# Kernel tuning notes

Hardware: AMD Instinct MI355X
Metric: run time of the kernel (lower is better)

## Reference

```python
import jax, jax.numpy as jnp
import numpy as np

N_NODES = 32768
N_EDGES = 262144
N_TYPES = 10
EMB = 16            # node_embedding_size, irreps_node_in = 16x0e
NB = 20             # num_basis = conv_radius * basis_density_per_A
RADIUS = 5.0        # conv_radius
S, V, T = 16, 4, 2  # output multiplicities for 0e, 1o, 2e
HID = 64
SILU_NORM = 1.679177  # e3nn normalize2mom constant for silu (E[silu(z)^2]^-0.5)


def _sph_harm(u):
    # e3nn real spherical harmonics, lmax=2, component normalization, unit input
    x, y, z = u[:, 0], u[:, 1], u[:, 2]
    sh0 = jnp.ones_like(x)[:, None]
    sh1 = np.sqrt(3.0) * u  # [E,3]
    s15 = np.sqrt(15.0)
    sh2 = jnp.stack([
        s15 * x * z,
        s15 * x * y,
        np.sqrt(5.0) * (y * y - 0.5 * (x * x + z * z)),
        s15 * y * z,
        (s15 / 2.0) * (z * z - x * x),
    ], axis=-1)  # [E,5]
    return jnp.concatenate([sh0, sh1, sh2], axis=-1)  # [E,9]


def _radial_emb(dist):
    # e3nn soft_one_hot_linspace, basis='smooth_finite', cutoff=True
    centers = np.linspace(0.0, RADIUS, NB + 2)[1:-1].astype(np.float32)
    step = centers[1] - centers[0]
    d = (dist[:, None] - centers) / step  # [E,NB]
    mask = jnp.abs(d) < 1.0
    ds = jnp.where(mask, d, 0.0)
    # 1.14136 * exp(2) * exp(-1/(1+d)) * exp(-1/(1-d)) inside |d|<1, else 0
    f = 1.14136 * jnp.exp(2.0 - 1.0 / (1.0 + ds) - 1.0 / (1.0 - ds))
    return jnp.where(mask, f, 0.0) * np.sqrt(float(NB))  # .mul(num_basis**0.5)


def setup_inputs() -> dict:
    key = jax.random.key(0)
    ks = jax.random.split(key, 7)
    x = jax.random.uniform(ks[0], (N_NODES, N_TYPES), dtype=jnp.float32)
    pos = jax.random.uniform(ks[1], (N_NODES, 3), dtype=jnp.float32) * 4.0
    edge_index = jax.random.randint(ks[2], (2, N_EDGES), 0, N_NODES)
    W_emb1 = jax.random.normal(ks[3], (N_TYPES, HID), dtype=jnp.float32)
    W_emb2 = jax.random.normal(ks[4], (HID, EMB), dtype=jnp.float32)
    W_tp1 = jax.random.normal(ks[5], (NB, HID), dtype=jnp.float32)
    W_tp2 = jax.random.normal(ks[6], (HID, EMB * (S + V + T)), dtype=jnp.float32)
    return {"x": x, "pos": pos, "edge_index": edge_index,
            "W_emb1": W_emb1, "W_emb2": W_emb2, "W_tp1": W_tp1, "W_tp2": W_tp2}


def reference(x, pos, edge_index, W_emb1, W_emb2, W_tp1, W_tp2):
    # e3nn FullyConnectedNet (act=None): pure linear with 1/sqrt(fan_in)
    node_emb = ((x @ W_emb1) / np.sqrt(float(N_TYPES))) @ W_emb2 / np.sqrt(float(HID))  # [N,16]

    src, dst = edge_index[0], edge_index[1]
    vec = pos[dst] - pos[src]                                   # [E,3]
    dist = jnp.sqrt(jnp.sum(vec * vec, axis=1) + 1e-12)         # [E]
    unit = vec / dist[:, None]

    sh = _sph_harm(unit)        # [E,9]
    demb = _radial_emb(dist)    # [E,NB]

    # e3nn FullyConnectedNet with normalized silu on hidden layer
    h = SILU_NORM * jax.nn.silu((demb @ W_tp1) / np.sqrt(float(NB)))
    w = (h @ W_tp2) / np.sqrt(float(HID))  # [E, 352] per-edge TP weights

    E = w.shape[0]
    Ws = w[:, : EMB * S].reshape(E, EMB, S)
    Wv = w[:, EMB * S: EMB * (S + V)].reshape(E, EMB, V)
    Wt = w[:, EMB * (S + V):].reshape(E, EMB, T)

    z = node_emb[src]            # [E,16] gathered source scalars
    inv = 1.0 / np.sqrt(float(EMB))  # path_weight * wigner3j for 0e x l -> l

    out_s = jnp.einsum('ei,eiu->eu', z, Ws) * sh[:, 0:1] * inv               # [E,16]
    out_v = (jnp.einsum('ei,eiu,em->eum', z, Wv, sh[:, 1:4]) * inv).reshape(E, V * 3)
    out_t = (jnp.einsum('ei,eiu,em->eum', z, Wt, sh[:, 4:9]) * inv).reshape(E, T * 5)
    tp = jnp.concatenate([out_s, out_v, out_t], axis=1)                      # [E,38]

    num_neighbors = N_EDGES / N_NODES
    messages = jax.ops.segment_sum(tp, dst, num_segments=N_NODES) / np.sqrt(num_neighbors)
    return jnp.concatenate([node_emb, messages], axis=1)  # [N, 16+38]
```

## Files before the change

kernel.cpp:

```cpp
#include <hip/hip_runtime.h>
#include <hip/hip_fp16.h>
#include <math.h>

#define N_NODES 32768
#define N_EDGES 262144
#define OUTC 54
#define TPW  40
#define TGRID 64
#define TENT 384
#define NBINS 1345
#define TBLOCKS 1365

__device__ __forceinline__ unsigned pkh(float a, float b) {
    auto r = __builtin_amdgcn_cvt_pkrtz(a, b);
    union { decltype(r) v; unsigned u; } cv;
    cv.v = r;
    return cv.u;
}

__global__ __launch_bounds__(256) void node_emb_kernel(
    const float* __restrict__ x, const float* __restrict__ W1,
    const float* __restrict__ W2, float* __restrict__ out,
    float* __restrict__ znode)
{
    int n = blockIdx.x * blockDim.x + threadIdx.x;
    if (n >= N_NODES) return;
    const float inv10 = 0.31622776601683794f;
    const float inv64 = 0.125f;

    float xr[10];
    #pragma unroll
    for (int i = 0; i < 10; ++i) xr[i] = x[n*10 + i];

    float t[64];
    #pragma unroll
    for (int k = 0; k < 64; ++k) {
        float acc = 0.f;
        #pragma unroll
        for (int i = 0; i < 10; ++i) acc = fmaf(xr[i], W1[i*64 + k], acc);
        t[k] = acc * inv10;
    }

    float e[16];
    #pragma unroll
    for (int j = 0; j < 16; ++j) e[j] = 0.f;
    #pragma unroll
    for (int k = 0; k < 64; ++k) {
        float tk = t[k];
        #pragma unroll
        for (int j = 0; j < 16; ++j) e[j] = fmaf(tk, W2[k*16 + j], e[j]);
    }
    float4* zb = (float4*)(znode + (size_t)n * 16);
    #pragma unroll
    for (int q = 0; q < 4; ++q) {
        float4 v = make_float4(e[q*4+0]*inv64, e[q*4+1]*inv64,
                               e[q*4+2]*inv64, e[q*4+3]*inv64);
        zb[q] = v;
        out[n*OUTC + q*4 + 0] = v.x;
        out[n*OUTC + q*4 + 1] = v.y;
        out[n*OUTC + q*4 + 2] = v.z;
        out[n*OUTC + q*4 + 3] = v.w;
    }
}

__global__ __launch_bounds__(256) void prep_kernel(
    const float* __restrict__ Wt1, const float* __restrict__ Wt2,
    float* __restrict__ T,
    const int* __restrict__ ei, const float* __restrict__ pos,
    int* __restrict__ cd, int* __restrict__ cb, int* __restrict__ ebin,
    float4* __restrict__ evec)
{
    __shared__ int hist[NBINS];
    __shared__ float h[64];
    int t = threadIdx.x;

    if (blockIdx.x < TBLOCKS) {
        int entry = blockIdx.x;
        int m = entry / 65;
        int g = entry - m * 65;
        float d0 = (float)g * (1.0f / TGRID);
        float d1 = d0 - 1.0f;
        int j0 = m - 1, j1 = m;
        const float sq20 = 4.47213595499958f;

        float f0 = 0.f, f1 = 0.f;
        if (j0 >= 0 && j0 < 20)
            f0 = 1.14136f * expf(2.0f - 1.0f/(1.0f + d0) - 1.0f/(1.0f - d0)) * sq20;
        if (j1 >= 0 && j1 < 20)
            f1 = 1.14136f * expf(2.0f - 1.0f/(1.0f + d1) - 1.0f/(1.0f - d1)) * sq20;
        j0 = j0 < 0 ? 0 : (j0 > 19 ? 19 : j0);
        j1 = j1 < 0 ? 0 : (j1 > 19 ? 19 : j1);

        if (t < 64) {
            float a = fmaf(f0, Wt1[j0*64 + t], f1 * Wt1[j1*64 + t])
                      * 0.22360679774997896f;
            h[t] = 1.679177f * a / (1.0f + expf(-a));
        }
        __syncthreads();

        const float sc = 0.011048543456039806f;
        for (int e2 = t; e2 < TENT; e2 += 256) {
            int i = e2 / 24;
            int c = e2 - i * 24;
            float v = 0.f;
            if (c < 22) {
                int widx = (c < 16) ? (i*16 + c)
                         : (c < 20) ? (256 + i*4 + (c - 16))
                                    : (320 + i*2 + (c - 20));
                for (int k = 0; k < 64; ++k)
                    v = fmaf(h[k], Wt2[k*352 + widx], v);
                v *= sc;
            }
            T[(size_t)entry * TENT + e2] = v;
        }
    } else {
        for (int b = t; b < NBINS; b += 256) hist[b] = 0;
        __syncthreads();

        int e = (blockIdx.x - TBLOCKS) * 256 + t;
        int s = ei[e];
        int d = ei[N_EDGES + e];
        float px = pos[d*3+0] - pos[s*3+0];
        float py = pos[d*3+1] - pos[s*3+1];
        float pz = pos[d*3+2] - pos[s*3+2];
        float dist = sqrtf(px*px + py*py + pz*pz + 1e-12f);
        float rinv = 1.0f / dist;
        float tt = dist * 4.2f;
        evec[e] = make_float4(px*rinv, py*rinv, pz*rinv, tt);

        int bin;
        if (!(tt < 21.0f)) {
            bin = NBINS - 1;
        } else {
            int m = (int)tt;
            float gf = (tt - (float)m) * (float)TGRID;
            int g0 = (int)gf; if (g0 > TGRID-1) g0 = TGRID-1;
            bin = m * TGRID + g0;
            atomicAdd(&cd[d], 1);
        }
        ebin[e] = bin;
        atomicAdd(&hist[bin], 1);
        __syncthreads();

        for (int b = t; b < NBINS; b += 256) {
            int c = hist[b];
            if (c) atomicAdd(&cb[b], c);
        }
    }
}

__global__ __launch_bounds__(1024) void scan2_kernel(
    int* __restrict__ c0, int* __restrict__ s0arr,
    int* __restrict__ c1, int* __restrict__ s1arr)
{
    int* cursor = (blockIdx.x == 0) ? c0 : c1;
    int* start  = (blockIdx.x == 0) ? s0arr : s1arr;
    __shared__ int partial[1024];
    int tid = threadIdx.x;
    int base = tid * 32;
    int v[32];
    int s = 0;
    #pragma unroll
    for (int j = 0; j < 32; ++j) { v[j] = cursor[base + j]; s += v[j]; }
    partial[tid] = s;
    __syncthreads();
    for (int off = 1; off < 1024; off <<= 1) {
        int t = (tid >= off) ? partial[tid - off] : 0;
        __syncthreads();
        partial[tid] += t;
        __syncthreads();
    }
    int run = (tid > 0) ? partial[tid - 1] : 0;
    #pragma unroll
    for (int j = 0; j < 32; ++j) {
        start[base + j] = run;
        cursor[base + j] = run;
        run += v[j];
    }
    if (tid == 1023) start[32768] = run;
}

__global__ __launch_bounds__(256) void fill_bins_kernel(
    const int* __restrict__ ebin, const int* __restrict__ ei,
    int* __restrict__ cursor_bin,
    int4* __restrict__ binfo)
{
    __shared__ int hist[NBINS];
    __shared__ int rbase[NBINS];
    for (int b = threadIdx.x; b < NBINS; b += 256) hist[b] = 0;
    __syncthreads();

    int e = blockIdx.x * 256 + threadIdx.x;
    int bin = ebin[e];
    atomicAdd(&hist[bin], 1);
    __syncthreads();

    for (int b = threadIdx.x; b < NBINS; b += 256) {
        int c = hist[b];
        if (c) rbase[b] = atomicAdd(&cursor_bin[b], c);
        hist[b] = 0;
    }
    __syncthreads();

    int lr = atomicAdd(&hist[bin], 1);
    int slot = rbase[bin] + lr;
    binfo[slot] = make_int4(e, ei[e], ei[N_EDGES + e], 0);
}

__global__ __launch_bounds__(256) void edge_table_binned(
    const float4* __restrict__ evec,
    const float* __restrict__ T, const float* __restrict__ znode,
    const int4* __restrict__ binfo,
    unsigned short* __restrict__ tp, int* __restrict__ cursor,
    int2* __restrict__ elist2)
{
    int idx = blockIdx.x * 256 + threadIdx.x;
    int4 bf = binfo[idx];
    int e   = bf.x;
    int src = bf.y;
    int dst = bf.z;

    float4 ev = evec[e];
    float tt = ev.w;
    if (!(tt < 21.0f)) return;

    int slot = atomicAdd(&cursor[dst], 1);
    elist2[slot] = make_int2(e, idx);

    uint4* d4 = (uint4*)(tp + (size_t)idx * TPW);

    float ux = ev.x, uy = ev.y, uz = ev.z;

    int m  = (int)tt;
    float d0 = tt - (float)m;
    float gf = d0 * (float)TGRID;
    int g0 = (int)gf; if (g0 > TGRID-1) g0 = TGRID-1;
    float fr = gf - (float)g0;

    const float4* r0 = (const float4*)(T + (size_t)(m*65 + g0) * TENT);
    const float4* r1 = r0 + (TENT/4);

    const float4* zp = (const float4*)(znode + (size_t)src * 16);
    float4 zq0 = zp[0], zq1 = zp[1], zq2 = zp[2], zq3 = zp[3];
    float z[16] = {zq0.x, zq0.y, zq0.z, zq0.w,
                   zq1.x, zq1.y, zq1.z, zq1.w,
                   zq2.x, zq2.y, zq2.z, zq2.w,
                   zq3.x, zq3.y, zq3.z, zq3.w};

    float acc[24];
    #pragma unroll
    for (int c = 0; c < 24; ++c) acc[c] = 0.f;

    #pragma unroll
    for (int i = 0; i < 16; ++i) {
        float zi = z[i];
        #pragma unroll
        for (int q = 0; q < 6; ++q) {
            float4 v0 = r0[i*6 + q];
            float4 v1 = r1[i*6 + q];
            float w;
            w = fmaf(fr, v1.x - v0.x, v0.x); acc[q*4+0] = fmaf(zi, w, acc[q*4+0]);
            w = fmaf(fr, v1.y - v0.y, v0.y); acc[q*4+1] = fmaf(zi, w, acc[q*4+1]);
            w = fmaf(fr, v1.z - v0.z, v0.z); acc[q*4+2] = fmaf(zi, w, acc[q*4+2]);
            w = fmaf(fr, v1.w - v0.w, v0.w); acc[q*4+3] = fmaf(zi, w, acc[q*4+3]);
        }
    }

    float vals[38];
    #pragma unroll
    for (int c = 0; c < 22; ++c) vals[c] = acc[c];

    const float s3  = 1.7320508075688772f;
    const float s15 = 3.872983346207417f;
    const float s5  = 2.23606797749979f;
    float sh1x = s3*ux, sh1y = s3*uy, sh1z = s3*uz;
    float sh2a = s15 * ux * uz;
    float sh2b = s15 * ux * uy;
    float sh2c = s5 * (uy*uy - 0.5f*(ux*ux + uz*uz));
    float sh2d = s15 * uy * uz;
    float sh2e = 0.5f * s15 * (uz*uz - ux*ux);

    #pragma unroll
    for (int u = 1; u >= 0; --u) {
        float v = vals[20 + u];
        vals[28 + u*5 + 0] = v * sh2a;
        vals[28 + u*5 + 1] = v * sh2b;
        vals[28 + u*5 + 2] = v * sh2c;
        vals[28 + u*5 + 3] = v * sh2d;
        vals[28 + u*5 + 4] = v * sh2e;
    }
    #pragma unroll
    for (int u = 3; u >= 0; --u) {
        float v = vals[16 + u];
        vals[16 + u*3 + 0] = v * sh1x;
        vals[16 + u*3 + 1] = v * sh1y;
        vals[16 + u*3 + 2] = v * sh1z;
    }

    d4[0] = make_uint4(pkh(vals[0], vals[1]),  pkh(vals[2], vals[3]),
                       pkh(vals[4], vals[5]),  pkh(vals[6], vals[7]));
    d4[1] = make_uint4(pkh(vals[8], vals[9]),  pkh(vals[10], vals[11]),
                       pkh(vals[12], vals[13]),pkh(vals[14], vals[15]));
    d4[2] = make_uint4(pkh(vals[16], vals[17]),pkh(vals[18], vals[19]),
                       pkh(vals[20], vals[21]),pkh(vals[22], vals[23]));
    d4[3] = make_uint4(pkh(vals[24], vals[25]),pkh(vals[26], vals[27]),
                       pkh(vals[28], vals[29]),pkh(vals[30], vals[31]));
    d4[4] = make_uint4(pkh(vals[32], vals[33]),pkh(vals[34], vals[35]),
                       pkh(vals[36], vals[37]),0);
}

__global__ __launch_bounds__(256) void gather_sorted_kernel(
    const unsigned short* __restrict__ tp, const int* __restrict__ start,
    const int2* __restrict__ elist2, float* __restrict__ out)
{
    __shared__ int sid[4][128];
    __shared__ int srw[4][128];
    __shared__ int so[4][128];
    int wave = threadIdx.x >> 6;
    int lane = threadIdx.x & 63;
    int n = blockIdx.x * 4 + wave;
    int s0 = start[n], s1 = start[n+1];
    int K = s1 - s0;
    bool small = (K <= 128);

    if (small) {
        for (int j = lane; j < K; j += 64) {
            int2 v = elist2[s0 + j];
            sid[wave][j] = v.x;
            srw[wave][j] = v.y;
        }
    }
    __syncthreads();
    if (small) {
        for (int j = lane; j < K; j += 64) {
            int v = sid[wave][j];
            int r = 0;
            for (int q = 0; q < K; ++q) r += (sid[wave][q] < v);
            so[wave][r] = srw[wave][j];
        }
    }
    __syncthreads();

    if (lane < 19) {
        float acc0 = 0.f, acc1 = 0.f;
        if (small) {
            for (int j = 0; j < K; ++j) {
                const unsigned* row = (const unsigned*)
                    (tp + (size_t)so[wave][j] * TPW);
                unsigned v = row[lane];
                acc0 += __half2float(__ushort_as_half((unsigned short)(v & 0xffffu)));
                acc1 += __half2float(__ushort_as_half((unsigned short)(v >> 16)));
            }
        } else {
            for (int j = s0; j < s1; ++j) {
                int2 ev = elist2[j];
                const unsigned* row = (const unsigned*)
                    (tp + (size_t)ev.y * TPW);
                unsigned v = row[lane];
                acc0 += __half2float(__ushort_as_half((unsigned short)(v & 0xffffu)));
                acc1 += __half2float(__ushort_as_half((unsigned short)(v >> 16)));
            }
        }
        out[n*OUTC + 16 + 2*lane] = acc0;
        out[n*OUTC + 16 + 2*lane + 1] = acc1;
    }
}

__global__ __launch_bounds__(256) void edge_kernel_atomic(
    const float* __restrict__ pos, const int* __restrict__ ei,
    const float* __restrict__ Wt1, const float* __restrict__ Wt2,
    float* out)
{
    int e = blockIdx.x * blockDim.x + threadIdx.x;
    if (e >= N_EDGES) return;
    int src = ei[e];
    int dst = ei[N_EDGES + e];
    float px = pos[dst*3+0] - pos[src*3+0];
    float py = pos[dst*3+1] - pos[src*3+1];
    float pz = pos[dst*3+2] - pos[src*3+2];
    float dist = sqrtf(px*px + py*py + pz*pz + 1e-12f);
    float rinv = 1.0f / dist;
    float ux = px*rinv, uy = py*rinv, uz = pz*rinv;
    const float step = 5.0f / 21.0f;
    float tt = dist / step;
    int m  = (int)floorf(tt);
    int j0 = m - 1, j1 = m;
    float d0 = tt - (float)m, d1 = d0 - 1.0f;
    const float sq20 = 4.47213595499958f;
    float f0 = 0.f, f1 = 0.f;
    if (j0 >= 0 && j0 < 20)
        f0 = 1.14136f * expf(2.0f - 1.0f/(1.0f + d0) - 1.0f/(1.0f - d0)) * sq20;
    if (j1 >= 0 && j1 < 20 && d1 > -1.0f)
        f1 = 1.14136f * expf(2.0f - 1.0f/(1.0f + d1) - 1.0f/(1.0f - d1)) * sq20;
    if (f0 == 0.f && f1 == 0.f) return;
    j0 = j0 < 0 ? 0 : (j0 > 19 ? 19 : j0);
    j1 = j1 < 0 ? 0 : (j1 > 19 ? 19 : j1);
    const float* w1a = Wt1 + j0*64;
    const float* w1b = Wt1 + j1*64;
    float z[16];
    #pragma unroll
    for (int i = 0; i < 16; ++i) z[i] = out[src*OUTC + i];
    const float rsq20 = 0.22360679774997896f;
    const float snorm = 1.679177f;
    float accS[16], accV[4], accT[2];
    #pragma unroll
    for (int u = 0; u < 16; ++u) accS[u] = 0.f;
    #pragma unroll
    for (int u = 0; u < 4; ++u) accV[u] = 0.f;
    #pragma unroll
    for (int u = 0; u < 2; ++u) accT[u] = 0.f;
    for (int k = 0; k < 64; ++k) {
        float a = fmaf(f0, w1a[k], f1 * w1b[k]) * rsq20;
        float hk = snorm * a / (1.0f + expf(-a));
        const float* row = Wt2 + k*352;
        float tmp[16];
        #pragma unroll
        for (int u = 0; u < 16; ++u) tmp[u] = 0.f;
        #pragma unroll
        for (int i = 0; i < 16; ++i) {
            float zi = z[i];
            #pragma unroll
            for (int u = 0; u < 16; ++u) tmp[u] = fmaf(zi, row[i*16 + u], tmp[u]);
        }
        #pragma unroll
        for (int u = 0; u < 16; ++u) accS[u] = fmaf(hk, tmp[u], accS[u]);
        float tv[4] = {0.f,0.f,0.f,0.f};
        #pragma unroll
        for (int i = 0; i < 16; ++i) {
            float zi = z[i];
            #pragma unroll
            for (int u = 0; u < 4; ++u) tv[u] = fmaf(zi, row[256 + i*4 + u], tv[u]);
        }
        #pragma unroll
        for (int u = 0; u < 4; ++u) accV[u] = fmaf(hk, tv[u], accV[u]);
        float tw[2] = {0.f,0.f};
        #pragma unroll
        for (int i = 0; i < 16; ++i) {
            float zi = z[i];
            #pragma unroll
            for (int u = 0; u < 2; ++u) tw[u] = fmaf(zi, row[320 + i*2 + u], tw[u]);
        }
        #pragma unroll
        for (int u = 0; u < 2; ++u) accT[u] = fmaf(hk, tw[u], accT[u]);
    }
    const float sc = 0.125f * 0.25f * 0.35355339059327373f;
    const float s3  = 1.7320508075688772f;
    const float s15 = 3.872983346207417f;
    const float s5  = 2.23606797749979f;
    float sh1x = s3*ux, sh1y = s3*uy, sh1z = s3*uz;
    float sh2[5];
    sh2[0] = s15 * ux * uz;
    sh2[1] = s15 * ux * uy;
    sh2[2] = s5 * (uy*uy - 0.5f*(ux*ux + uz*uz));
    sh2[3] = s15 * uy * uz;
    sh2[4] = 0.5f * s15 * (uz*uz - ux*ux);
    float* orow = out + dst*OUTC + 16;
    #pragma unroll
    for (int u = 0; u < 16; ++u) atomicAdd(&orow[u], accS[u] * sc);
    #pragma unroll
    for (int u = 0; u < 4; ++u) {
        float v = accV[u] * sc;
        atomicAdd(&orow[16 + u*3 + 0], v * sh1x);
        atomicAdd(&orow[16 + u*3 + 1], v * sh1y);
        atomicAdd(&orow[16 + u*3 + 2], v * sh1z);
    }
    #pragma unroll
    for (int u = 0; u < 2; ++u) {
        float v = accT[u] * sc;
        #pragma unroll
        for (int mm = 0; mm < 5; ++mm)
            atomicAdd(&orow[28 + u*5 + mm], v * sh2[mm]);
    }
}

extern "C" void kernel_launch(void* const* d_in, const int* in_sizes, int n_in,
                              void* d_out, int out_size, void* d_ws, size_t ws_size,
                              hipStream_t stream) {
    const float* x   = (const float*)d_in[0];
    const float* pos = (const float*)d_in[1];
    const int*   ei  = (const int*)d_in[2];
    const float* We1 = (const float*)d_in[3];
    const float* We2 = (const float*)d_in[4];
    const float* Wt1 = (const float*)d_in[5];
    const float* Wt2 = (const float*)d_in[6];
    float* out = (float*)d_out;

    char* base = (char*)d_ws;
    size_t off = 0;
    unsigned short* tp = (unsigned short*)(base + off);
    off += (size_t)N_EDGES * TPW * 2;
    float* T  = (float*)(base + off);       off += (size_t)TBLOCKS * TENT * 4;
    float* znode = (float*)(base + off);    off += (size_t)N_NODES * 16 * 4;
    float4* evec = (float4*)(base + off);   off += (size_t)N_EDGES * 16;
    int* cursor_dst = (int*)(base + off);   off += (size_t)32768 * 4;
    int* cursor_bin = (int*)(base + off);   off += (size_t)32768 * 4;
    int* start_dst  = (int*)(base + off);   off += (size_t)32769 * 4;
    int* start_bin  = (int*)(base + off);   off += (size_t)32769 * 4;
    int* ebin       = (int*)(base + off);   off += (size_t)N_EDGES * 4;
    int4* binfo     = (int4*)(base + off);  off += (size_t)N_EDGES * 16;
    int2* elist2    = (int2*)(base + off);  off += (size_t)N_EDGES * 8;
    size_t need = off;

    if (ws_size >= need) {
        node_emb_kernel<<<N_NODES/256, 256, 0, stream>>>(x, We1, We2, out, znode);
        hipMemsetAsync(cursor_dst, 0, (size_t)2 * 32768 * 4, stream);
        prep_kernel<<<TBLOCKS + N_EDGES/256, 256, 0, stream>>>(
            Wt1, Wt2, T, ei, pos, cursor_dst, cursor_bin, ebin, evec);
        scan2_kernel<<<2, 1024, 0, stream>>>(cursor_dst, start_dst,
                                             cursor_bin, start_bin);
        fill_bins_kernel<<<N_EDGES/256, 256, 0, stream>>>(ebin, ei, cursor_bin,
                                                          binfo);
        edge_table_binned<<<N_EDGES/256, 256, 0, stream>>>(evec, T, znode,
                                                           binfo, tp,
                                                           cursor_dst, elist2);
        gather_sorted_kernel<<<N_NODES/4, 256, 0, stream>>>(tp, start_dst,
                                                            elist2, out);
    } else {
        hipMemsetAsync(out, 0, (size_t)out_size * sizeof(float), stream);
        node_emb_kernel<<<N_NODES/256, 256, 0, stream>>>(x, We1, We2, out,
                                                         (float*)d_ws);
        edge_kernel_atomic<<<N_EDGES/256, 256, 0, stream>>>(pos, ei, Wt1, Wt2, out);
    }
}
```

Before: 175.5 us.

## Fuse node embedding into prep kernel, compact table rows, co-sort edge vectors

The node-embedding launch is folded into prep_kernel as a third block range, with the edge-geometry blocks reordered to run first. The radial weight table drops its padded 24-wide interleaved layout for the natural 352-entry weight order, which shrinks table rows and the reads in edge_table_binned. fill_bins also writes each edge's unit vector and distance into a bin-sorted array, so the edge kernel reads it contiguously instead of gathering by edge id. This costs an extra 4 MB scatter write and uses float2 and unaligned-stride loads on the table.

```diff
diff --git a/kernel.cpp b/kernel.cpp
--- a/kernel.cpp
+++ b/kernel.cpp
@@ -7,9 +7,11 @@
 #define OUTC 54
 #define TPW  40
 #define TGRID 64
-#define TENT 384
+#define TENT 352
 #define NBINS 1345
 #define TBLOCKS 1365
+#define CBLK (N_EDGES/256)
+#define NBLK (N_NODES/256)
 
 __device__ __forceinline__ unsigned pkh(float a, float b) {
     auto r = __builtin_amdgcn_cvt_pkrtz(a, b);
@@ -18,13 +20,11 @@
     return cv.u;
 }
 
-__global__ __launch_bounds__(256) void node_emb_kernel(
-    const float* __restrict__ x, const float* __restrict__ W1,
+__device__ __forceinline__ void node_emb_body(
+    int n, const float* __restrict__ x, const float* __restrict__ W1,
     const float* __restrict__ W2, float* __restrict__ out,
     float* __restrict__ znode)
 {
-    int n = blockIdx.x * blockDim.x + threadIdx.x;
-    if (n >= N_NODES) return;
     const float inv10 = 0.31622776601683794f;
     const float inv64 = 0.125f;
 
@@ -63,61 +63,34 @@
     }
 }
 
+__global__ __launch_bounds__(256) void node_emb_kernel(
+    const float* __restrict__ x, const float* __restrict__ W1,
+    const float* __restrict__ W2, float* __restrict__ out,
+    float* __restrict__ znode)
+{
+    int n = blockIdx.x * blockDim.x + threadIdx.x;
+    if (n < N_NODES) node_emb_body(n, x, W1, W2, out, znode);
+}
+
 __global__ __launch_bounds__(256) void prep_kernel(
     const float* __restrict__ Wt1, const float* __restrict__ Wt2,
     float* __restrict__ T,
     const int* __restrict__ ei, const float* __restrict__ pos,
     int* __restrict__ cd, int* __restrict__ cb, int* __restrict__ ebin,
-    float4* __restrict__ evec)
+    float4* __restrict__ evec,
+    const float* __restrict__ x, const float* __restrict__ We1,
+    const float* __restrict__ We2, float* __restrict__ out,
+    float* __restrict__ znode)
 {
     __shared__ int hist[NBINS];
     __shared__ float h[64];
     int t = threadIdx.x;
 
-    if (blockIdx.x < TBLOCKS) {
-        int entry = blockIdx.x;
-        int m = entry / 65;
-        int g = entry - m * 65;
-        float d0 = (float)g * (1.0f / TGRID);
-        float d1 = d0 - 1.0f;
-        int j0 = m - 1, j1 = m;
-        const float sq20 = 4.47213595499958f;
-
-        float f0 = 0.f, f1 = 0.f;
-        if (j0 >= 0 && j0 < 20)
-            f0 = 1.14136f * expf(2.0f - 1.0f/(1.0f + d0) - 1.0f/(1.0f - d0)) * sq20;
-        if (j1 >= 0 && j1 < 20)
-            f1 = 1.14136f * expf(2.0f - 1.0f/(1.0f + d1) - 1.0f/(1.0f - d1)) * sq20;
-        j0 = j0 < 0 ? 0 : (j0 > 19 ? 19 : j0);
-        j1 = j1 < 0 ? 0 : (j1 > 19 ? 19 : j1);
-
-        if (t < 64) {
-            float a = fmaf(f0, Wt1[j0*64 + t], f1 * Wt1[j1*64 + t])
-                      * 0.22360679774997896f;
-            h[t] = 1.679177f * a / (1.0f + expf(-a));
-        }
-        __syncthreads();
-
-        const float sc = 0.011048543456039806f;
-        for (int e2 = t; e2 < TENT; e2 += 256) {
-            int i = e2 / 24;
-            int c = e2 - i * 24;
-            float v = 0.f;
-            if (c < 22) {
-                int widx = (c < 16) ? (i*16 + c)
-                         : (c < 20) ? (256 + i*4 + (c - 16))
-                                    : (320 + i*2 + (c - 20));
-                for (int k = 0; k < 64; ++k)
-                    v = fmaf(h[k], Wt2[k*352 + widx], v);
-                v *= sc;
-            }
-            T[(size_t)entry * TENT + e2] = v;
-        }
-    } else {
+    if (blockIdx.x < CBLK) {
         for (int b = t; b < NBINS; b += 256) hist[b] = 0;
         __syncthreads();
 
-        int e = (blockIdx.x - TBLOCKS) * 256 + t;
+        int e = blockIdx.x * 256 + t;
         int s = ei[e];
         int d = ei[N_EDGES + e];
         float px = pos[d*3+0] - pos[s*3+0];
@@ -146,6 +119,40 @@
             int c = hist[b];
             if (c) atomicAdd(&cb[b], c);
         }
+    } else if (blockIdx.x < CBLK + TBLOCKS) {
+        int entry = blockIdx.x - CBLK;
+        int m = entry / 65;
+        int g = entry - m * 65;
+        float d0 = (float)g * (1.0f / TGRID);
+        float d1 = d0 - 1.0f;
+        int j0 = m - 1, j1 = m;
+        const float sq20 = 4.47213595499958f;
+
+        float f0 = 0.f, f1 = 0.f;
+        if (j0 >= 0 && j0 < 20)
+            f0 = 1.14136f * expf(2.0f - 1.0f/(1.0f + d0) - 1.0f/(1.0f - d0)) * sq20;
+        if (j1 >= 0 && j1 < 20)
+            f1 = 1.14136f * expf(2.0f - 1.0f/(1.0f + d1) - 1.0f/(1.0f - d1)) * sq20;
+        j0 = j0 < 0 ? 0 : (j0 > 19 ? 19 : j0);
+        j1 = j1 < 0 ? 0 : (j1 > 19 ? 19 : j1);
+
+        if (t < 64) {
+            float a = fmaf(f0, Wt1[j0*64 + t], f1 * Wt1[j1*64 + t])
+                      * 0.22360679774997896f;
+            h[t] = 1.679177f * a / (1.0f + expf(-a));
+        }
+        __syncthreads();
+
+        const float sc = 0.011048543456039806f;
+        for (int widx = t; widx < TENT; widx += 256) {
+            float v = 0.f;
+            for (int k = 0; k < 64; ++k)
+                v = fmaf(h[k], Wt2[k*352 + widx], v);
+            T[(size_t)entry * TENT + widx] = v * sc;
+        }
+    } else {
+        int n = (blockIdx.x - CBLK - TBLOCKS) * 256 + t;
+        node_emb_body(n, x, We1, We2, out, znode);
     }
 }
 
@@ -182,8 +189,9 @@
 
 __global__ __launch_bounds__(256) void fill_bins_kernel(
     const int* __restrict__ ebin, const int* __restrict__ ei,
+    const float4* __restrict__ evec,
     int* __restrict__ cursor_bin,
-    int4* __restrict__ binfo)
+    int4* __restrict__ binfoA, float4* __restrict__ binfoB)
 {
     __shared__ int hist[NBINS];
     __shared__ int rbase[NBINS];
@@ -204,23 +212,23 @@
 
     int lr = atomicAdd(&hist[bin], 1);
     int slot = rbase[bin] + lr;
-    binfo[slot] = make_int4(e, ei[e], ei[N_EDGES + e], 0);
+    binfoA[slot] = make_int4(e, ei[e], ei[N_EDGES + e], 0);
+    binfoB[slot] = evec[e];
 }
 
 __global__ __launch_bounds__(256) void edge_table_binned(
-    const float4* __restrict__ evec,
     const float* __restrict__ T, const float* __restrict__ znode,
-    const int4* __restrict__ binfo,
+    const int4* __restrict__ binfoA, const float4* __restrict__ binfoB,
     unsigned short* __restrict__ tp, int* __restrict__ cursor,
     int2* __restrict__ elist2)
 {
     int idx = blockIdx.x * 256 + threadIdx.x;
-    int4 bf = binfo[idx];
+    int4 bf = binfoA[idx];
     int e   = bf.x;
     int src = bf.y;
     int dst = bf.z;
 
-    float4 ev = evec[e];
+    float4 ev = binfoB[idx];
     float tt = ev.w;
     if (!(tt < 21.0f)) return;
 
@@ -237,8 +245,8 @@
     int g0 = (int)gf; if (g0 > TGRID-1) g0 = TGRID-1;
     float fr = gf - (float)g0;
 
-    const float4* r0 = (const float4*)(T + (size_t)(m*65 + g0) * TENT);
-    const float4* r1 = r0 + (TENT/4);
+    const float* r0 = T + (size_t)(m*65 + g0) * TENT;
+    const float* r1 = r0 + TENT;
 
     const float4* zp = (const float4*)(znode + (size_t)src * 16);
     float4 zq0 = zp[0], zq1 = zp[1], zq2 = zp[2], zq3 = zp[3];
@@ -247,22 +255,38 @@
                    zq2.x, zq2.y, zq2.z, zq2.w,
                    zq3.x, zq3.y, zq3.z, zq3.w};
 
-    float acc[24];
-    #pragma unroll
-    for (int c = 0; c < 24; ++c) acc[c] = 0.f;
+    float acc[22];
+    #pragma unroll
+    for (int c = 0; c < 22; ++c) acc[c] = 0.f;
 
     #pragma unroll
     for (int i = 0; i < 16; ++i) {
         float zi = z[i];
         #pragma unroll
-        for (int q = 0; q < 6; ++q) {
-            float4 v0 = r0[i*6 + q];
-            float4 v1 = r1[i*6 + q];
+        for (int q = 0; q < 4; ++q) {
+            float4 v0 = *(const float4*)(r0 + i*16 + q*4);
+            float4 v1 = *(const float4*)(r1 + i*16 + q*4);
             float w;
             w = fmaf(fr, v1.x - v0.x, v0.x); acc[q*4+0] = fmaf(zi, w, acc[q*4+0]);
             w = fmaf(fr, v1.y - v0.y, v0.y); acc[q*4+1] = fmaf(zi, w, acc[q*4+1]);
             w = fmaf(fr, v1.z - v0.z, v0.z); acc[q*4+2] = fmaf(zi, w, acc[q*4+2]);
             w = fmaf(fr, v1.w - v0.w, v0.w); acc[q*4+3] = fmaf(zi, w, acc[q*4+3]);
+        }
+        {
+            float4 v0 = *(const float4*)(r0 + 256 + i*4);
+            float4 v1 = *(const float4*)(r1 + 256 + i*4);
+            float w;
+            w = fmaf(fr, v1.x - v0.x, v0.x); acc[16] = fmaf(zi, w, acc[16]);
+            w = fmaf(fr, v1.y - v0.y, v0.y); acc[17] = fmaf(zi, w, acc[17]);
+            w = fmaf(fr, v1.z - v0.z, v0.z); acc[18] = fmaf(zi, w, acc[18]);
+            w = fmaf(fr, v1.w - v0.w, v0.w); acc[19] = fmaf(zi, w, acc[19]);
+        }
+        {
+            float2 t0 = *(const float2*)(r0 + 320 + i*2);
+            float2 t1 = *(const float2*)(r1 + 320 + i*2);
+            float w;
+            w = fmaf(fr, t1.x - t0.x, t0.x); acc[20] = fmaf(zi, w, acc[20]);
+            w = fmaf(fr, t1.y - t0.y, t0.y); acc[21] = fmaf(zi, w, acc[21]);
         }
     }
 
@@ -497,21 +521,23 @@
     int* start_dst  = (int*)(base + off);   off += (size_t)32769 * 4;
     int* start_bin  = (int*)(base + off);   off += (size_t)32769 * 4;
     int* ebin       = (int*)(base + off);   off += (size_t)N_EDGES * 4;
-    int4* binfo     = (int4*)(base + off);  off += (size_t)N_EDGES * 16;
+    int4* binfoA    = (int4*)(base + off);  off += (size_t)N_EDGES * 16;
+    float4* binfoB  = (float4*)(base + off); off += (size_t)N_EDGES * 16;
     int2* elist2    = (int2*)(base + off);  off += (size_t)N_EDGES * 8;
     size_t need = off;
 
     if (ws_size >= need) {
-        node_emb_kernel<<<N_NODES/256, 256, 0, stream>>>(x, We1, We2, out, znode);
         hipMemsetAsync(cursor_dst, 0, (size_t)2 * 32768 * 4, stream);
-        prep_kernel<<<TBLOCKS + N_EDGES/256, 256, 0, stream>>>(
-            Wt1, Wt2, T, ei, pos, cursor_dst, cursor_bin, ebin, evec);
+        prep_kernel<<<CBLK + TBLOCKS + NBLK, 256, 0, stream>>>(
+            Wt1, Wt2, T, ei, pos, cursor_dst, cursor_bin, ebin, evec,
+            x, We1, We2, out, znode);
         scan2_kernel<<<2, 1024, 0, stream>>>(cursor_dst, start_dst,
                                              cursor_bin, start_bin);
-        fill_bins_kernel<<<N_EDGES/256, 256, 0, stream>>>(ebin, ei, cursor_bin,
-                                                          binfo);
-        edge_table_binned<<<N_EDGES/256, 256, 0, stream>>>(evec, T, znode,
-                                                           binfo, tp,
+        fill_bins_kernel<<<N_EDGES/256, 256, 0, stream>>>(ebin, ei, evec,
+                                                          cursor_bin,
+                                                          binfoA, binfoB);
+        edge_table_binned<<<N_EDGES/256, 256, 0, stream>>>(T, znode,
+                                                           binfoA, binfoB, tp,
                                                            cursor_dst, elist2);
         gather_sorted_kernel<<<N_NODES/4, 256, 0, stream>>>(tp, start_dst,
                                                             elist2, out);
```

Result: slower. 183.8 us (+4.7%).
